# Optimization experiments

Hardware: AMD Instinct MI355X
Metric: run time of the kernel (lower is better)

The kernel has to match this reference:

```python
import jax, jax.numpy as jnp
import numpy as np

NUM_HEADS = 16
THETA = 10000.0
B, S, D = 2, 2048, 1024
D_K = D // NUM_HEADS


def setup_inputs() -> dict:
    key = jax.random.key(0)
    ks = jax.random.split(key, 5)
    s = 0.02
    return {
        "x": jax.random.normal(ks[0], (B, S, D), dtype=jnp.float32),
        "W_q": jax.random.normal(ks[1], (D, D), dtype=jnp.float32) * s,
        "W_k": jax.random.normal(ks[2], (D, D), dtype=jnp.float32) * s,
        "W_v": jax.random.normal(ks[3], (D, D), dtype=jnp.float32) * s,
        "W_o": jax.random.normal(ks[4], (D, D), dtype=jnp.float32) * s,
        "token_positions": jnp.arange(S, dtype=jnp.int32),
    }


def _rope(x, token_positions):
    # x: [..., seq, d_k]; equivalent to the block-diagonal 2x2 rotation matmul
    d2 = x.shape[-1] // 2
    inv_freq = THETA ** (-(2.0 * jnp.arange(d2, dtype=x.dtype)) / x.shape[-1])  # [d2]
    ang = token_positions.astype(x.dtype)[:, None] * inv_freq[None, :]  # [seq, d2]
    cos, sin = jnp.cos(ang), jnp.sin(ang)
    xp = x.reshape(x.shape[:-1] + (d2, 2))
    xe, xo = xp[..., 0], xp[..., 1]
    oe = cos * xe - sin * xo
    oo = sin * xe + cos * xo
    return jnp.stack([oe, oo], axis=-1).reshape(x.shape)


def reference(x, W_q, W_k, W_v, W_o, token_positions):
    seq = x.shape[-2]
    # QKV projections (weights stored as [out, in])
    Q = jnp.einsum('bsd,ed->bse', x, W_q)
    K = jnp.einsum('bsd,ed->bse', x, W_k)
    V = jnp.einsum('bsd,ed->bse', x, W_v)
    def split_heads(t):
        return t.reshape(t.shape[:-1] + (NUM_HEADS, D_K)).swapaxes(-3, -2)  # [b,h,s,dk]
    Q, K, V = split_heads(Q), split_heads(K), split_heads(V)
    Q = _rope(Q, token_positions)
    K = _rope(K, token_positions)
    scale = 1.0 / np.sqrt(D_K)
    scores = jnp.einsum('bhqd,bhkd->bhqk', Q, K) * scale
    causal = jnp.tril(jnp.ones((seq, seq), dtype=bool))
    scores = jnp.where(causal, scores, -jnp.inf)
    probs = jax.nn.softmax(scores, axis=-1)
    out = jnp.einsum('bhqk,bhkd->bhqd', probs, V)
    out = out.swapaxes(-3, -2).reshape(x.shape[:-1] + (D,))
    return jnp.einsum('bse,de->bsd', out, W_o)
```

## Files before the change

kernel.cpp:

```cpp
#include <hip/hip_runtime.h>
#include <hip/hip_bf16.h>
#include <math.h>

#define H_    16
#define DK_   64
#define Dm    1024
#define Bb    2
#define Ss    2048
#define Mrows 4096
#define QSCALE 0.1803368801f

typedef short s16x8 __attribute__((ext_vector_type(8)));
typedef float f32x4 __attribute__((ext_vector_type(4)));
typedef unsigned short u16;
typedef unsigned int u32;

__device__ __forceinline__ u16 f2b(float f) {
  __hip_bfloat16 h = __float2bfloat16(f);
  return *reinterpret_cast<u16*>(&h);
}
__device__ __forceinline__ float b2f(u16 u) {
  __hip_bfloat16 h;
  *reinterpret_cast<u16*>(&h) = u;
  return __bfloat162float(h);
}
__device__ __forceinline__ u32 pkbf(float hi, float lo) {
  return __builtin_amdgcn_perm(__float_as_uint(hi), __float_as_uint(lo), 0x07060302u);
}

#define GLDS(g, l)                                                             \
  __builtin_amdgcn_global_load_lds(                                            \
      (const __attribute__((address_space(1))) unsigned int*)(g),              \
      (__attribute__((address_space(3))) unsigned int*)(l), 16, 0, 0)

__device__ __forceinline__ int SW64(int row, int col) {
  return row * 64 + ((((col >> 3) ^ (row & 7) ^ (row >> 3)) & 7) << 3) + (col & 7);
}

__global__ __launch_bounds__(256) void k_castall(
    const float* __restrict__ x,  const float* __restrict__ Wq,
    const float* __restrict__ Wk, const float* __restrict__ Wv,
    const float* __restrict__ Wo,
    u16* __restrict__ xb,  u16* __restrict__ wqb, u16* __restrict__ wkb,
    u16* __restrict__ wvb, u16* __restrict__ wob) {
  int i = blockIdx.x * 256 + threadIdx.x;
  const float* s;
  u16* d;
  int off;
  if (i < 1048576) { s = x; d = xb; off = i; }
  else {
    int j = i - 1048576;
    int w = j >> 18;
    off = j & 262143;
    s = (w == 0) ? Wq : (w == 1) ? Wk : (w == 2) ? Wv : Wo;
    d = (w == 0) ? wqb : (w == 1) ? wkb : (w == 2) ? wvb : wob;
  }
  float4 v = reinterpret_cast<const float4*>(s)[off];
  ushort4 o;
  o.x = f2b(v.x); o.y = f2b(v.y); o.z = f2b(v.z); o.w = f2b(v.w);
  reinterpret_cast<ushort4*>(d)[off] = o;
}

__global__ __launch_bounds__(256) void k_ropetab(const int* __restrict__ pos,
                                                 float2* __restrict__ tab) {
  int t = blockIdx.x * 256 + threadIdx.x;
  int s = t >> 5, i = t & 31;
  float p = (float)pos[s];
  float ang = p * powf(10000.0f, -(float)i / 32.0f);
  tab[t] = make_float2(cosf(ang), sinf(ang));
}

__global__ __launch_bounds__(256) void k_rope2(u16* __restrict__ Q, u16* __restrict__ K,
                                               const float2* __restrict__ tab) {
  int t = blockIdx.x * 256 + threadIdx.x;
  int row = t >> 7;
  int c0 = (t & 127) << 3;
  int i0 = (c0 & 63) >> 1;
  const float2* tb = &tab[(row & (Ss - 1)) * 32 + i0];
  float2 cs[4];
#pragma unroll
  for (int j = 0; j < 4; ++j) cs[j] = tb[j];
  size_t off = (size_t)row * Dm + c0;
  s16x8 q = *reinterpret_cast<const s16x8*>(&Q[off]);
  s16x8 k = *reinterpret_cast<const s16x8*>(&K[off]);
  s16x8 qo, ko;
#pragma unroll
  for (int j = 0; j < 4; ++j) {
    float qe = b2f((u16)q[2 * j]), qd = b2f((u16)q[2 * j + 1]);
    qo[2 * j]     = (short)f2b((cs[j].x * qe - cs[j].y * qd) * QSCALE);
    qo[2 * j + 1] = (short)f2b((cs[j].y * qe + cs[j].x * qd) * QSCALE);
    float ke = b2f((u16)k[2 * j]), kd = b2f((u16)k[2 * j + 1]);
    ko[2 * j]     = (short)f2b(cs[j].x * ke - cs[j].y * kd);
    ko[2 * j + 1] = (short)f2b(cs[j].y * ke + cs[j].x * kd);
  }
  *reinterpret_cast<s16x8*>(&Q[off]) = qo;
  *reinterpret_cast<s16x8*>(&K[off]) = ko;
}

template <int BN, bool QKV>
__global__ __launch_bounds__(256) void k_gemm(
    const u16* __restrict__ A, const u16* __restrict__ B,
    u16* __restrict__ OQ, u16* __restrict__ OK2, u16* __restrict__ OVT,
    float* __restrict__ OF, int K) {
  constexpr int NFR = BN / 32;
  __shared__ __align__(16) u16 lsA[2][128 * 64];
  __shared__ __align__(16) u16 lsB[2][BN * 64];
  const int tid = threadIdx.x, lane = tid & 63, wave = tid >> 6;
  const int quad = lane >> 4, l16 = lane & 15;
  const int wrow = wave >> 1, wcol = wave & 1;
  const int n0 = blockIdx.x * BN, m0 = blockIdx.y * 128;
  f32x4 acc[4][NFR] = {};

  auto stage = [&](int k0, int bi) {
#pragma unroll
    for (int c = 0; c < 4; ++c) {
      int slot = (wave * 4 + c) * 64 + lane;
      int row = slot >> 3;
      int gg = ((slot & 7) ^ (row & 7) ^ (row >> 3)) & 7;
      GLDS(A + (size_t)(m0 + row) * K + k0 + gg * 8, &lsA[bi][(wave * 4 + c) * 512]);
    }
#pragma unroll
    for (int c = 0; c < NFR; ++c) {
      int cc = wave * NFR + c;
      int slot = cc * 64 + lane;
      int row = slot >> 3;
      int gg = ((slot & 7) ^ (row & 7) ^ (row >> 3)) & 7;
      GLDS(B + (size_t)(n0 + row) * K + k0 + gg * 8, &lsB[bi][cc * 512]);
    }
  };

  stage(0, 0);
  int bi = 0;
  for (int k0 = 0; k0 < K; k0 += 64) {
    __syncthreads();
    if (k0 + 64 < K) stage(k0 + 64, bi ^ 1);
#pragma unroll
    for (int kc = 0; kc < 2; ++kc) {
      s16x8 af[4], bfr[NFR];
#pragma unroll
      for (int i = 0; i < 4; ++i)
        af[i] = *reinterpret_cast<const s16x8*>(
            &lsA[bi][SW64(wrow * 64 + i * 16 + l16, kc * 32 + quad * 8)]);
#pragma unroll
      for (int i = 0; i < NFR; ++i)
        bfr[i] = *reinterpret_cast<const s16x8*>(
            &lsB[bi][SW64(wcol * (BN / 2) + i * 16 + l16, kc * 32 + quad * 8)]);
#pragma unroll
      for (int mi = 0; mi < 4; ++mi)
#pragma unroll
        for (int ni = 0; ni < NFR; ++ni)
          acc[mi][ni] = __builtin_amdgcn_mfma_f32_16x16x32_bf16(af[mi], bfr[ni], acc[mi][ni], 0, 0, 0);
    }
    bi ^= 1;
  }

  if (QKV) {
    const int which = n0 >> 10;
    const int nbase = (n0 & 1023) + wcol * (BN / 2);
    if (which == 2) {
#pragma unroll
      for (int mi = 0; mi < 4; ++mi)
#pragma unroll
        for (int ni = 0; ni < NFR; ++ni) {
          int row0 = m0 + wrow * 64 + mi * 16 + quad * 4;
          int col  = nbase + ni * 16 + l16;
          int bb = row0 >> 11, s0 = row0 & (Ss - 1);
          ushort4 pk;
          pk.x = f2b(acc[mi][ni][0]); pk.y = f2b(acc[mi][ni][1]);
          pk.z = f2b(acc[mi][ni][2]); pk.w = f2b(acc[mi][ni][3]);
          *reinterpret_cast<ushort4*>(&OVT[((size_t)bb * Dm + col) * Ss + s0]) = pk;
        }
    } else {
      u16* Op = which ? OK2 : OQ;
#pragma unroll
      for (int mi = 0; mi < 4; ++mi)
#pragma unroll
        for (int ni = 0; ni < NFR; ++ni)
#pragma unroll
          for (int r = 0; r < 4; ++r) {
            int row = m0 + wrow * 64 + mi * 16 + quad * 4 + r;
            int col = nbase + ni * 16 + l16;
            Op[(size_t)row * Dm + col] = f2b(acc[mi][ni][r]);
          }
    }
  } else {
#pragma unroll
    for (int mi = 0; mi < 4; ++mi)
#pragma unroll
      for (int ni = 0; ni < NFR; ++ni)
#pragma unroll
        for (int r = 0; r < 4; ++r) {
          int row = m0 + wrow * 64 + mi * 16 + quad * 4 + r;
          int col = n0 + wcol * (BN / 2) + ni * 16 + l16;
          OF[(size_t)row * Dm + col] = acc[mi][ni][r];
        }
  }
}

__global__ __launch_bounds__(256) void k_flash(const u16* __restrict__ Q,
                                               const u16* __restrict__ K,
                                               const u16* __restrict__ VT,
                                               u16* __restrict__ O) {
  __shared__ __align__(16) u16 lsK[2][64 * 64];
  __shared__ __align__(16) u16 lsVT[2][64 * 64];
  __shared__ __align__(16) u16 lsP[4][32 * 64];
  const int tid = threadIdx.x, lane = tid & 63, wave = tid >> 6;
  const int quad = lane >> 4, l16 = lane & 15;
  const int bid = blockIdx.x;
  const int bh = bid & 31;
  const int h = bh & (H_ - 1), b = bh >> 4;
  const int g = bid >> 5, a = g & 7, bsel = g >> 3;
  const int qt = bsel ? (15 - a) : a;
  const int q0 = qt * 128;
  const int qbase = q0 + wave * 32;
  const int ktmax_w = (qbase + 31) >> 6;
  const int ktmax_b = 2 * qt + 1;
  const int xorv = (l16 * 2) & 0xE;

  s16x8 qf[2][2];
#pragma unroll
  for (int s = 0; s < 2; ++s) {
    const size_t qoff = (size_t)(b * Ss + qbase + s * 16 + l16) * Dm + h * 64;
    qf[s][0] = *reinterpret_cast<const s16x8*>(&Q[qoff + quad * 8]);
    qf[s][1] = *reinterpret_cast<const s16x8*>(&Q[qoff + 32 + quad * 8]);
  }
  s16x8 ones;
#pragma unroll
  for (int j = 0; j < 8; ++j) ones[j] = (short)0x3F80;

  f32x4 ot[2][4] = {};
  f32x4 lAcc[2] = {};

  auto stage = [&](int kt, int bi) {
    const size_t kbase  = (size_t)(b * Ss + kt * 64) * Dm + h * 64;
    const size_t vtbase = ((size_t)b * Dm + h * 64) * Ss + kt * 64;
#pragma unroll
    for (int c = 0; c < 2; ++c) {
      int slot = (wave * 2 + c) * 64 + lane;
      int row = slot >> 3;
      int gg = ((slot & 7) ^ (row & 7) ^ (row >> 3)) & 7;
      GLDS(K  + kbase  + (size_t)row * Dm + gg * 8, &lsK[bi][(wave * 2 + c) * 512]);
      GLDS(VT + vtbase + (size_t)row * Ss + gg * 8, &lsVT[bi][(wave * 2 + c) * 512]);
    }
  };

  stage(0, 0);
  for (int kt = 0; kt <= ktmax_b; ++kt) {
    __syncthreads();
    if (kt < ktmax_b) stage(kt + 1, (kt + 1) & 1);
    if (kt > ktmax_w) continue;
    const int bi = kt & 1;

    f32x4 st[2][4] = {};
#pragma unroll
    for (int kc = 0; kc < 2; ++kc)
#pragma unroll
      for (int ni = 0; ni < 4; ++ni) {
        s16x8 kf = *reinterpret_cast<const s16x8*>(
            &lsK[bi][SW64(ni * 16 + l16, kc * 32 + quad * 8)]);
        st[0][ni] = __builtin_amdgcn_mfma_f32_16x16x32_bf16(kf, qf[0][kc], st[0][ni], 0, 0, 0);
        st[1][ni] = __builtin_amdgcn_mfma_f32_16x16x32_bf16(kf, qf[1][kc], st[1][ni], 0, 0, 0);
      }
    if (kt == ktmax_w) {
#pragma unroll
      for (int s = 0; s < 2; ++s) {
        int gq = qbase + s * 16 + l16;
#pragma unroll
        for (int ni = 0; ni < 4; ++ni)
#pragma unroll
          for (int r = 0; r < 4; ++r)
            if (kt * 64 + ni * 16 + quad * 4 + r > gq) st[s][ni][r] = -INFINITY;
      }
    }
#pragma unroll
    for (int s = 0; s < 2; ++s)
#pragma unroll
      for (int ni = 0; ni < 4; ++ni) {
        float e0 = __builtin_amdgcn_exp2f(st[s][ni][0]);
        float e1 = __builtin_amdgcn_exp2f(st[s][ni][1]);
        float e2 = __builtin_amdgcn_exp2f(st[s][ni][2]);
        float e3 = __builtin_amdgcn_exp2f(st[s][ni][3]);
        uint2 pk;
        pk.x = pkbf(e1, e0);
        pk.y = pkbf(e3, e2);
        *reinterpret_cast<uint2*>(
            &lsP[wave][(s * 16 + l16) * 64 + (((ni * 4 + quad) ^ xorv) << 2)]) = pk;
      }
#pragma unroll
    for (int kc = 0; kc < 2; ++kc) {
      s16x8 pf0 = *reinterpret_cast<const s16x8*>(
          &lsP[wave][l16 * 64 + (((kc * 8 + quad * 2) ^ xorv) << 2)]);
      s16x8 pf1 = *reinterpret_cast<const s16x8*>(
          &lsP[wave][(16 + l16) * 64 + (((kc * 8 + quad * 2) ^ xorv) << 2)]);
      lAcc[0] = __builtin_amdgcn_mfma_f32_16x16x32_bf16(ones, pf0, lAcc[0], 0, 0, 0);
      lAcc[1] = __builtin_amdgcn_mfma_f32_16x16x32_bf16(ones, pf1, lAcc[1], 0, 0, 0);
#pragma unroll
      for (int ni = 0; ni < 4; ++ni) {
        s16x8 vf = *reinterpret_cast<const s16x8*>(
            &lsVT[bi][SW64(ni * 16 + l16, kc * 32 + quad * 8)]);
        ot[0][ni] = __builtin_amdgcn_mfma_f32_16x16x32_bf16(vf, pf0, ot[0][ni], 0, 0, 0);
        ot[1][ni] = __builtin_amdgcn_mfma_f32_16x16x32_bf16(vf, pf1, ot[1][ni], 0, 0, 0);
      }
    }
  }

#pragma unroll
  for (int s = 0; s < 2; ++s) {
    float inv = 1.0f / lAcc[s][0];
    const size_t obase = (size_t)(b * Ss + qbase + s * 16 + l16) * Dm + h * 64;
#pragma unroll
    for (int ni = 0; ni < 4; ++ni) {
      ushort4 pk;
      pk.x = f2b(ot[s][ni][0] * inv); pk.y = f2b(ot[s][ni][1] * inv);
      pk.z = f2b(ot[s][ni][2] * inv); pk.w = f2b(ot[s][ni][3] * inv);
      *reinterpret_cast<ushort4*>(&O[obase + ni * 16 + quad * 4]) = pk;
    }
  }
}

extern "C" void kernel_launch(void* const* d_in, const int* in_sizes, int n_in,
                              void* d_out, int out_size, void* d_ws, size_t ws_size,
                              hipStream_t stream) {
  const float* x  = (const float*)d_in[0];
  const float* Wq = (const float*)d_in[1];
  const float* Wk = (const float*)d_in[2];
  const float* Wv = (const float*)d_in[3];
  const float* Wo = (const float*)d_in[4];
  const int* pos  = (const int*)d_in[5];
  float* out = (float*)d_out;

  char* w = (char*)d_ws;
  u16* xb  = (u16*)w; w += (size_t)Mrows * Dm * 2;
  u16* wqb = (u16*)w; w += (size_t)Dm * Dm * 2;
  u16* wkb = (u16*)w; w += (size_t)Dm * Dm * 2;
  u16* wvb = (u16*)w; w += (size_t)Dm * Dm * 2;
  u16* wob = (u16*)w; w += (size_t)Dm * Dm * 2;
  u16* Qb  = (u16*)w; w += (size_t)Mrows * Dm * 2;
  u16* Kb  = (u16*)w; w += (size_t)Mrows * Dm * 2;
  u16* VTb = (u16*)w; w += (size_t)Mrows * Dm * 2;
  u16* Ab  = (u16*)w; w += (size_t)Mrows * Dm * 2;
  float2* tabf = (float2*)w; w += (size_t)Ss * 32 * sizeof(float2);

  k_castall<<<8192, 256, 0, stream>>>(x, Wq, Wk, Wv, Wo, xb, wqb, wkb, wvb, wob);
  k_ropetab<<<Ss * 32 / 256, 256, 0, stream>>>(pos, tabf);

  k_gemm<128, true><<<dim3(24, 32), 256, 0, stream>>>(xb, wqb, Qb, Kb, VTb, nullptr, Dm);
  k_rope2<<<Mrows * Dm / 8 / 256, 256, 0, stream>>>(Qb, Kb, tabf);
  k_flash<<<dim3(512), 256, 0, stream>>>(Qb, Kb, VTb, Ab);
  k_gemm<64, false><<<dim3(16, 32), 256, 0, stream>>>(Ab, wob, nullptr, nullptr, nullptr, out, Dm);
}
```

Before: 196.5 us.

## Fuse Q RoPE into flash load, merge rope table into cast, stage KV pairs

Folds the RoPE-table computation into the cast kernel, which removes one launch. Q's rotation and scaling move into the flash kernel's Q-fragment load, so the separate rope pass now rewrites only K and the global Q read-modify-write is gone. The flash loop now stages two K/V tiles per barrier into a 4-slot LDS ring, which halves the number of __syncthreads per tile. The cost is twice the K/V LDS footprint, which may lower occupancy, plus more registers for the doubled score accumulators.

```diff
diff --git a/kernel.cpp b/kernel.cpp
--- a/kernel.cpp
+++ b/kernel.cpp
@@ -42,7 +42,16 @@
     const float* __restrict__ Wk, const float* __restrict__ Wv,
     const float* __restrict__ Wo,
     u16* __restrict__ xb,  u16* __restrict__ wqb, u16* __restrict__ wkb,
-    u16* __restrict__ wvb, u16* __restrict__ wob) {
+    u16* __restrict__ wvb, u16* __restrict__ wob,
+    const int* __restrict__ pos, float2* __restrict__ tab) {
+  if (blockIdx.x >= 8192) {
+    int t = (blockIdx.x - 8192) * 256 + threadIdx.x;
+    int s = t >> 5, i = t & 31;
+    float p = (float)pos[s];
+    float ang = p * powf(10000.0f, -(float)i / 32.0f);
+    tab[t] = make_float2(cosf(ang), sinf(ang));
+    return;
+  }
   int i = blockIdx.x * 256 + threadIdx.x;
   const float* s;
   u16* d;
@@ -61,16 +70,7 @@
   reinterpret_cast<ushort4*>(d)[off] = o;
 }
 
-__global__ __launch_bounds__(256) void k_ropetab(const int* __restrict__ pos,
-                                                 float2* __restrict__ tab) {
-  int t = blockIdx.x * 256 + threadIdx.x;
-  int s = t >> 5, i = t & 31;
-  float p = (float)pos[s];
-  float ang = p * powf(10000.0f, -(float)i / 32.0f);
-  tab[t] = make_float2(cosf(ang), sinf(ang));
-}
-
-__global__ __launch_bounds__(256) void k_rope2(u16* __restrict__ Q, u16* __restrict__ K,
+__global__ __launch_bounds__(256) void k_ropeK(u16* __restrict__ K,
                                                const float2* __restrict__ tab) {
   int t = blockIdx.x * 256 + threadIdx.x;
   int row = t >> 7;
@@ -81,19 +81,14 @@
 #pragma unroll
   for (int j = 0; j < 4; ++j) cs[j] = tb[j];
   size_t off = (size_t)row * Dm + c0;
-  s16x8 q = *reinterpret_cast<const s16x8*>(&Q[off]);
   s16x8 k = *reinterpret_cast<const s16x8*>(&K[off]);
-  s16x8 qo, ko;
+  s16x8 ko;
 #pragma unroll
   for (int j = 0; j < 4; ++j) {
-    float qe = b2f((u16)q[2 * j]), qd = b2f((u16)q[2 * j + 1]);
-    qo[2 * j]     = (short)f2b((cs[j].x * qe - cs[j].y * qd) * QSCALE);
-    qo[2 * j + 1] = (short)f2b((cs[j].y * qe + cs[j].x * qd) * QSCALE);
     float ke = b2f((u16)k[2 * j]), kd = b2f((u16)k[2 * j + 1]);
     ko[2 * j]     = (short)f2b(cs[j].x * ke - cs[j].y * kd);
     ko[2 * j + 1] = (short)f2b(cs[j].y * ke + cs[j].x * kd);
   }
-  *reinterpret_cast<s16x8*>(&Q[off]) = qo;
   *reinterpret_cast<s16x8*>(&K[off]) = ko;
 }
 
@@ -200,9 +195,10 @@
 __global__ __launch_bounds__(256) void k_flash(const u16* __restrict__ Q,
                                                const u16* __restrict__ K,
                                                const u16* __restrict__ VT,
-                                               u16* __restrict__ O) {
-  __shared__ __align__(16) u16 lsK[2][64 * 64];
-  __shared__ __align__(16) u16 lsVT[2][64 * 64];
+                                               u16* __restrict__ O,
+                                               const float2* __restrict__ tab) {
+  __shared__ __align__(16) u16 lsK[4][64 * 64];
+  __shared__ __align__(16) u16 lsVT[4][64 * 64];
   __shared__ __align__(16) u16 lsP[4][32 * 64];
   const int tid = threadIdx.x, lane = tid & 63, wave = tid >> 6;
   const int quad = lane >> 4, l16 = lane & 15;
@@ -214,15 +210,27 @@
   const int q0 = qt * 128;
   const int qbase = q0 + wave * 32;
   const int ktmax_w = (qbase + 31) >> 6;
-  const int ktmax_b = 2 * qt + 1;
   const int xorv = (l16 * 2) & 0xE;
 
   s16x8 qf[2][2];
 #pragma unroll
   for (int s = 0; s < 2; ++s) {
-    const size_t qoff = (size_t)(b * Ss + qbase + s * 16 + l16) * Dm + h * 64;
-    qf[s][0] = *reinterpret_cast<const s16x8*>(&Q[qoff + quad * 8]);
-    qf[s][1] = *reinterpret_cast<const s16x8*>(&Q[qoff + 32 + quad * 8]);
+    const int qpos = qbase + s * 16 + l16;
+    const size_t qoff = (size_t)(b * Ss + qpos) * Dm + h * 64;
+    s16x8 r0 = *reinterpret_cast<const s16x8*>(&Q[qoff + quad * 8]);
+    s16x8 r1 = *reinterpret_cast<const s16x8*>(&Q[qoff + 32 + quad * 8]);
+    const float2* tb = &tab[(qpos & (Ss - 1)) * 32];
+#pragma unroll
+    for (int kc = 0; kc < 2; ++kc) {
+      s16x8 raw = kc ? r1 : r0;
+#pragma unroll
+      for (int p = 0; p < 4; ++p) {
+        float2 cs = tb[kc * 16 + quad * 4 + p];
+        float e = b2f((u16)raw[2 * p]), o = b2f((u16)raw[2 * p + 1]);
+        qf[s][kc][2 * p]     = (short)f2b((cs.x * e - cs.y * o) * QSCALE);
+        qf[s][kc][2 * p + 1] = (short)f2b((cs.y * e + cs.x * o) * QSCALE);
+      }
+    }
   }
   s16x8 ones;
 #pragma unroll
@@ -231,75 +239,91 @@
   f32x4 ot[2][4] = {};
   f32x4 lAcc[2] = {};
 
-  auto stage = [&](int kt, int bi) {
-    const size_t kbase  = (size_t)(b * Ss + kt * 64) * Dm + h * 64;
-    const size_t vtbase = ((size_t)b * Dm + h * 64) * Ss + kt * 64;
-#pragma unroll
-    for (int c = 0; c < 2; ++c) {
-      int slot = (wave * 2 + c) * 64 + lane;
-      int row = slot >> 3;
-      int gg = ((slot & 7) ^ (row & 7) ^ (row >> 3)) & 7;
-      GLDS(K  + kbase  + (size_t)row * Dm + gg * 8, &lsK[bi][(wave * 2 + c) * 512]);
-      GLDS(VT + vtbase + (size_t)row * Ss + gg * 8, &lsVT[bi][(wave * 2 + c) * 512]);
+  auto stagepair = [&](int pp) {
+#pragma unroll
+    for (int half = 0; half < 2; ++half) {
+      const int kt = pp * 2 + half;
+      const int slot = kt & 3;
+      const size_t kbase  = (size_t)(b * Ss + kt * 64) * Dm + h * 64;
+      const size_t vtbase = ((size_t)b * Dm + h * 64) * Ss + kt * 64;
+#pragma unroll
+      for (int c = 0; c < 2; ++c) {
+        int sl = (wave * 2 + c) * 64 + lane;
+        int row = sl >> 3;
+        int gg = ((sl & 7) ^ (row & 7) ^ (row >> 3)) & 7;
+        GLDS(K  + kbase  + (size_t)row * Dm + gg * 8, &lsK[slot][(wave * 2 + c) * 512]);
+        GLDS(VT + vtbase + (size_t)row * Ss + gg * 8, &lsVT[slot][(wave * 2 + c) * 512]);
+      }
     }
   };
 
-  stage(0, 0);
-  for (int kt = 0; kt <= ktmax_b; ++kt) {
+  stagepair(0);
+  for (int pp = 0; pp <= qt; ++pp) {
     __syncthreads();
-    if (kt < ktmax_b) stage(kt + 1, (kt + 1) & 1);
-    if (kt > ktmax_w) continue;
-    const int bi = kt & 1;
-
-    f32x4 st[2][4] = {};
-#pragma unroll
-    for (int kc = 0; kc < 2; ++kc)
-#pragma unroll
-      for (int ni = 0; ni < 4; ++ni) {
-        s16x8 kf = *reinterpret_cast<const s16x8*>(
-            &lsK[bi][SW64(ni * 16 + l16, kc * 32 + quad * 8)]);
-        st[0][ni] = __builtin_amdgcn_mfma_f32_16x16x32_bf16(kf, qf[0][kc], st[0][ni], 0, 0, 0);
-        st[1][ni] = __builtin_amdgcn_mfma_f32_16x16x32_bf16(kf, qf[1][kc], st[1][ni], 0, 0, 0);
+    if (pp < qt) stagepair(pp + 1);
+    const int kt0 = 2 * pp;
+
+    f32x4 st[2][2][4] = {};
+#pragma unroll
+    for (int half = 0; half < 2; ++half) {
+      const int kt = kt0 + half;
+      if (kt > ktmax_w) break;
+      const int slot = kt & 3;
+#pragma unroll
+      for (int kc = 0; kc < 2; ++kc)
+#pragma unroll
+        for (int ni = 0; ni < 4; ++ni) {
+          s16x8 kf = *reinterpret_cast<const s16x8*>(
+              &lsK[slot][SW64(ni * 16 + l16, kc * 32 + quad * 8)]);
+          st[half][0][ni] = __builtin_amdgcn_mfma_f32_16x16x32_bf16(kf, qf[0][kc], st[half][0][ni], 0, 0, 0);
+          st[half][1][ni] = __builtin_amdgcn_mfma_f32_16x16x32_bf16(kf, qf[1][kc], st[half][1][ni], 0, 0, 0);
+        }
+    }
+#pragma unroll
+    for (int half = 0; half < 2; ++half) {
+      const int kt = kt0 + half;
+      if (kt > ktmax_w) break;
+      const int slot = kt & 3;
+      if (kt == ktmax_w) {
+#pragma unroll
+        for (int s = 0; s < 2; ++s) {
+          int gq = qbase + s * 16 + l16;
+#pragma unroll
+          for (int ni = 0; ni < 4; ++ni)
+#pragma unroll
+            for (int r = 0; r < 4; ++r)
+              if (kt * 64 + ni * 16 + quad * 4 + r > gq) st[half][s][ni][r] = -INFINITY;
+        }
       }
-    if (kt == ktmax_w) {
-#pragma unroll
-      for (int s = 0; s < 2; ++s) {
-        int gq = qbase + s * 16 + l16;
-#pragma unroll
-        for (int ni = 0; ni < 4; ++ni)
-#pragma unroll
-          for (int r = 0; r < 4; ++r)
-            if (kt * 64 + ni * 16 + quad * 4 + r > gq) st[s][ni][r] = -INFINITY;
-      }
-    }
-#pragma unroll
-    for (int s = 0; s < 2; ++s)
-#pragma unroll
-      for (int ni = 0; ni < 4; ++ni) {
-        float e0 = __builtin_amdgcn_exp2f(st[s][ni][0]);
-        float e1 = __builtin_amdgcn_exp2f(st[s][ni][1]);
-        float e2 = __builtin_amdgcn_exp2f(st[s][ni][2]);
-        float e3 = __builtin_amdgcn_exp2f(st[s][ni][3]);
-        uint2 pk;
-        pk.x = pkbf(e1, e0);
-        pk.y = pkbf(e3, e2);
-        *reinterpret_cast<uint2*>(
-            &lsP[wave][(s * 16 + l16) * 64 + (((ni * 4 + quad) ^ xorv) << 2)]) = pk;
-      }
-#pragma unroll
-    for (int kc = 0; kc < 2; ++kc) {
-      s16x8 pf0 = *reinterpret_cast<const s16x8*>(
-          &lsP[wave][l16 * 64 + (((kc * 8 + quad * 2) ^ xorv) << 2)]);
-      s16x8 pf1 = *reinterpret_cast<const s16x8*>(
-          &lsP[wave][(16 + l16) * 64 + (((kc * 8 + quad * 2) ^ xorv) << 2)]);
-      lAcc[0] = __builtin_amdgcn_mfma_f32_16x16x32_bf16(ones, pf0, lAcc[0], 0, 0, 0);
-      lAcc[1] = __builtin_amdgcn_mfma_f32_16x16x32_bf16(ones, pf1, lAcc[1], 0, 0, 0);
-#pragma unroll
-      for (int ni = 0; ni < 4; ++ni) {
-        s16x8 vf = *reinterpret_cast<const s16x8*>(
-            &lsVT[bi][SW64(ni * 16 + l16, kc * 32 + quad * 8)]);
-        ot[0][ni] = __builtin_amdgcn_mfma_f32_16x16x32_bf16(vf, pf0, ot[0][ni], 0, 0, 0);
-        ot[1][ni] = __builtin_amdgcn_mfma_f32_16x16x32_bf16(vf, pf1, ot[1][ni], 0, 0, 0);
+#pragma unroll
+      for (int s = 0; s < 2; ++s)
+#pragma unroll
+        for (int ni = 0; ni < 4; ++ni) {
+          float e0 = __builtin_amdgcn_exp2f(st[half][s][ni][0]);
+          float e1 = __builtin_amdgcn_exp2f(st[half][s][ni][1]);
+          float e2 = __builtin_amdgcn_exp2f(st[half][s][ni][2]);
+          float e3 = __builtin_amdgcn_exp2f(st[half][s][ni][3]);
+          uint2 pk;
+          pk.x = pkbf(e1, e0);
+          pk.y = pkbf(e3, e2);
+          *reinterpret_cast<uint2*>(
+              &lsP[wave][(s * 16 + l16) * 64 + (((ni * 4 + quad) ^ xorv) << 2)]) = pk;
+        }
+#pragma unroll
+      for (int kc = 0; kc < 2; ++kc) {
+        s16x8 pf0 = *reinterpret_cast<const s16x8*>(
+            &lsP[wave][l16 * 64 + (((kc * 8 + quad * 2) ^ xorv) << 2)]);
+        s16x8 pf1 = *reinterpret_cast<const s16x8*>(
+            &lsP[wave][(16 + l16) * 64 + (((kc * 8 + quad * 2) ^ xorv) << 2)]);
+        lAcc[0] = __builtin_amdgcn_mfma_f32_16x16x32_bf16(ones, pf0, lAcc[0], 0, 0, 0);
+        lAcc[1] = __builtin_amdgcn_mfma_f32_16x16x32_bf16(ones, pf1, lAcc[1], 0, 0, 0);
+#pragma unroll
+        for (int ni = 0; ni < 4; ++ni) {
+          s16x8 vf = *reinterpret_cast<const s16x8*>(
+              &lsVT[slot][SW64(ni * 16 + l16, kc * 32 + quad * 8)]);
+          ot[0][ni] = __builtin_amdgcn_mfma_f32_16x16x32_bf16(vf, pf0, ot[0][ni], 0, 0, 0);
+          ot[1][ni] = __builtin_amdgcn_mfma_f32_16x16x32_bf16(vf, pf1, ot[1][ni], 0, 0, 0);
+        }
       }
     }
   }
@@ -341,11 +365,10 @@
   u16* Ab  = (u16*)w; w += (size_t)Mrows * Dm * 2;
   float2* tabf = (float2*)w; w += (size_t)Ss * 32 * sizeof(float2);
 
-  k_castall<<<8192, 256, 0, stream>>>(x, Wq, Wk, Wv, Wo, xb, wqb, wkb, wvb, wob);
-  k_ropetab<<<Ss * 32 / 256, 256, 0, stream>>>(pos, tabf);
-
+  k_castall<<<8448, 256, 0, stream>>>(x, Wq, Wk, Wv, Wo, xb, wqb, wkb, wvb, wob,
+                                      pos, tabf);
   k_gemm<128, true><<<dim3(24, 32), 256, 0, stream>>>(xb, wqb, Qb, Kb, VTb, nullptr, Dm);
-  k_rope2<<<Mrows * Dm / 8 / 256, 256, 0, stream>>>(Qb, Kb, tabf);
-  k_flash<<<dim3(512), 256, 0, stream>>>(Qb, Kb, VTb, Ab);
+  k_ropeK<<<Mrows * Dm / 8 / 256, 256, 0, stream>>>(Kb, tabf);
+  k_flash<<<dim3(512), 256, 0, stream>>>(Qb, Kb, VTb, Ab, tabf);
   k_gemm<64, false><<<dim3(16, 32), 256, 0, stream>>>(Ab, wob, nullptr, nullptr, nullptr, out, Dm);
 }
```

Result: faster. 190.2 us (-3.2%).
